# Optimization experiments

Measured on AMD Instinct MI355X. Metric: run time of the kernel, lower is better.

The kernel has to match this reference:

```python
import jax, jax.numpy as jnp
import numpy as np

B, L, D = 4096, 200, 128  # batch, neighbor bonds per molecule, bond feature dim
LN_EPS = 1e-5


def setup_inputs() -> dict:
    key = jax.random.key(0)
    ks = jax.random.split(key, 6)
    s = 1.0 / np.sqrt(D).astype(np.float32)
    return {
        "mol_bond_feature": jax.random.normal(ks[0], (B, D), jnp.float32),
        "bond_feature": jax.random.normal(ks[1], (B, L, D), jnp.float32),
        "mol_bond_attend_mask": jnp.ones((B, L, 1), jnp.float32),
        "mol_bond_softmax_mask": jnp.zeros((B, L, 1), jnp.float32),
        "W_self": jax.random.normal(ks[2], (D, D), jnp.float32) * s,   # mol_bond_fc
        "b_self": jnp.zeros((D,), jnp.float32),
        "W_nb": jax.random.normal(ks[3], (D, D), jnp.float32) * s,     # mol_bond_neighbor_fc
        "b_nb": jnp.zeros((D,), jnp.float32),
        "w_align": jax.random.normal(ks[4], (2 * D,), jnp.float32) * s,  # GAT align weight [2D]->1
        "b_align": jnp.zeros((), jnp.float32),
        "ln_gamma": jnp.ones((D,), jnp.float32),
        "ln_beta": jnp.zeros((D,), jnp.float32),
    }


def reference(mol_bond_feature, bond_feature, mol_bond_attend_mask,
              mol_bond_softmax_mask, W_self, b_self, W_nb, b_nb,
              w_align, b_align, ln_gamma, ln_beta):
    # Linear projections (dropout p=0 -> identity)
    x = mol_bond_feature @ W_self.T + b_self            # [B, D]
    y = jnp.einsum('bld,ed->ble', bond_feature, W_nb) + b_nb  # [B, L, D]

    # GAT align: Linear over concat([x_expand, y]) == split dot products (no concat materialized)
    wx, wy = w_align[:D], w_align[D:]
    score = (x @ wx)[:, None, None] + jnp.einsum('bld,d->bl', y, wy)[..., None] + b_align  # [B, L, 1]
    score = jax.nn.leaky_relu(score)                    # GNN_attn_act
    score = score + mol_bond_softmax_mask

    attn = jax.nn.softmax(score, axis=-2) * mol_bond_attend_mask  # [B, L, 1]
    ctx = jnp.sum(attn * y, axis=-2)                    # [B, D]

    # LayerNorm
    mu = jnp.mean(ctx, axis=-1, keepdims=True)
    var = jnp.mean(jnp.square(ctx - mu), axis=-1, keepdims=True)
    return (ctx - mu) * jax.lax.rsqrt(var + LN_EPS) * ln_gamma + ln_beta
```

## Files before the change

### kernel.cpp

```cpp
#include <hip/hip_runtime.h>
#include <math.h>

#define B_ 4096
#define L_ 200
#define D_ 128

__global__ void prep_kernel(const float* __restrict__ W_self,
                            const float* __restrict__ W_nb,
                            const float* __restrict__ b_self,
                            const float* __restrict__ b_nb,
                            const float* __restrict__ w_align,
                            const float* __restrict__ b_align,
                            float* __restrict__ ws) {
  int d = threadIdx.x;
  float su = 0.f, sv = 0.f;
  for (int e = 0; e < D_; ++e) {
    su = fmaf(w_align[e],      W_self[e * D_ + d], su);
    sv = fmaf(w_align[D_ + e], W_nb[e * D_ + d],   sv);
  }
  ws[d]      = su;
  ws[D_ + d] = sv;
  if (d == 0) {
    float cb = 0.f, cc = 0.f;
    for (int e = 0; e < D_; ++e) {
      cb = fmaf(b_self[e], w_align[e],      cb);
      cc = fmaf(b_nb[e],   w_align[D_ + e], cc);
    }
    ws[2 * D_]     = cb;
    ws[2 * D_ + 1] = cc + b_align[0];
  }
}

__global__ __launch_bounds__(256) void mol_bond_main(
    const float* __restrict__ mbf,
    const float* __restrict__ bond,
    const float* __restrict__ amask,
    const float* __restrict__ smask,
    const float* __restrict__ W_nb,
    const float* __restrict__ b_nb,
    const float* __restrict__ gamma,
    const float* __restrict__ beta,
    const float* __restrict__ ws,
    float* __restrict__ out) {
  const int b    = blockIdx.x;
  const int tid  = threadIdx.x;
  const int w    = tid >> 6;
  const int lane = tid & 63;
  const int half = lane >> 5;
  const int sl   = lane & 31;
  const int d0   = 4 * sl;

  __shared__ float am_s[L_];
  __shared__ float sm_s[L_];
  __shared__ float g_l[8][D_];
  __shared__ float sA[8][2];
  __shared__ float gfin[D_];
  __shared__ float ctx_l[D_];
  __shared__ float Afin_s;

  for (int l = tid; l < L_; l += 256) {
    am_s[l] = amask[(size_t)b * L_ + l];
    sm_s[l] = smask[(size_t)b * L_ + l];
  }

  const float4 uu = *(const float4*)(ws + d0);
  const float4 vv = *(const float4*)(ws + D_ + d0);
  const float  cb = ws[2 * D_], cc = ws[2 * D_ + 1];

  float4 mb = *(const float4*)(mbf + (size_t)b * D_ + d0);
  float xp = mb.x * uu.x + mb.y * uu.y + mb.z * uu.z + mb.w * uu.w;
  xp += __shfl_xor(xp, 16, 64);
  xp += __shfl_xor(xp, 8, 64);
  xp += __shfl_xor(xp, 4, 64);
  xp += __shfl_xor(xp, 2, 64);
  xp += __shfl_xor(xp, 1, 64);
  const float xs = xp + cb;

  __syncthreads();

  float s = 0.f, A = 0.f;
  float g0 = 0.f, g1 = 0.f, g2 = 0.f, g3 = 0.f;
  const float* bb = bond + (size_t)b * (L_ * D_);

  int l = w * 2 + half;
  #pragma unroll 5
  for (int it = 0; it < L_ / 8; ++it, l += 8) {
    float4 f = *(const float4*)(bb + l * D_ + d0);
    float t = f.x * vv.x + f.y * vv.y + f.z * vv.z + f.w * vv.w;
    t += __shfl_xor(t, 16, 64);
    t += __shfl_xor(t, 8, 64);
    t += __shfl_xor(t, 4, 64);
    t += __shfl_xor(t, 2, 64);
    t += __shfl_xor(t, 1, 64);
    float sc = xs + t + cc;
    sc = sc >= 0.f ? sc : 0.01f * sc;
    sc += sm_s[l];
    float p  = __expf(sc);
    float pa = p * am_s[l];
    s += p;
    A += pa;
    g0 = fmaf(pa, f.x, g0);
    g1 = fmaf(pa, f.y, g1);
    g2 = fmaf(pa, f.z, g2);
    g3 = fmaf(pa, f.w, g3);
  }
  const int st = w * 2 + half;
  *(float4*)(&g_l[st][d0]) = make_float4(g0, g1, g2, g3);
  if (sl == 0) { sA[st][0] = s; sA[st][1] = A; }
  __syncthreads();

  if (tid < D_) {
    float gs = 0.f, stot = 0.f, At = 0.f;
    #pragma unroll
    for (int k = 0; k < 8; ++k) {
      gs   += g_l[k][tid];
      stot += sA[k][0];
      At   += sA[k][1];
    }
    float inv = 1.0f / stot;
    gfin[tid] = gs * inv;
    if (tid == 0) Afin_s = At * inv;
  }
  __syncthreads();

  if (tid < D_) {
    const int e = tid;
    const float4* Wr = (const float4*)(W_nb + (size_t)e * D_);
    float acc = b_nb[e] * Afin_s;
    #pragma unroll 8
    for (int k = 0; k < D_ / 4; ++k) {
      float4 wv = Wr[k];
      acc += wv.x * gfin[4 * k]     + wv.y * gfin[4 * k + 1]
           + wv.z * gfin[4 * k + 2] + wv.w * gfin[4 * k + 3];
    }
    ctx_l[e] = acc;
  }
  __syncthreads();

  if (tid < 64) {
    float c0 = ctx_l[lane], c1 = ctx_l[lane + 64];
    float t0 = c0 + c1;
    t0 += __shfl_xor(t0, 32, 64);
    t0 += __shfl_xor(t0, 16, 64);
    t0 += __shfl_xor(t0, 8, 64);
    t0 += __shfl_xor(t0, 4, 64);
    t0 += __shfl_xor(t0, 2, 64);
    t0 += __shfl_xor(t0, 1, 64);
    float mu = t0 * (1.0f / 128.0f);
    float dd0 = c0 - mu, dd1 = c1 - mu;
    float v0 = dd0 * dd0 + dd1 * dd1;
    v0 += __shfl_xor(v0, 32, 64);
    v0 += __shfl_xor(v0, 16, 64);
    v0 += __shfl_xor(v0, 8, 64);
    v0 += __shfl_xor(v0, 4, 64);
    v0 += __shfl_xor(v0, 2, 64);
    v0 += __shfl_xor(v0, 1, 64);
    float var = v0 * (1.0f / 128.0f);
    float inv = rsqrtf(var + 1e-5f);
    out[(size_t)b * D_ + lane]      = dd0 * inv * gamma[lane]      + beta[lane];
    out[(size_t)b * D_ + lane + 64] = dd1 * inv * gamma[lane + 64] + beta[lane + 64];
  }
}

extern "C" void kernel_launch(void* const* d_in, const int* in_sizes, int n_in,
                              void* d_out, int out_size, void* d_ws, size_t ws_size,
                              hipStream_t stream) {
  const float* mbf     = (const float*)d_in[0];
  const float* bond    = (const float*)d_in[1];
  const float* amask   = (const float*)d_in[2];
  const float* smask   = (const float*)d_in[3];
  const float* W_self  = (const float*)d_in[4];
  const float* b_self  = (const float*)d_in[5];
  const float* W_nb    = (const float*)d_in[6];
  const float* b_nb    = (const float*)d_in[7];
  const float* w_align = (const float*)d_in[8];
  const float* b_align = (const float*)d_in[9];
  const float* gamma   = (const float*)d_in[10];
  const float* beta    = (const float*)d_in[11];
  float* ws  = (float*)d_ws;
  float* out = (float*)d_out;

  prep_kernel<<<1, D_, 0, stream>>>(W_self, W_nb, b_self, b_nb, w_align, b_align, ws);
  mol_bond_main<<<B_, 256, 0, stream>>>(mbf, bond, amask, smask, W_nb, b_nb,
                                        gamma, beta, ws, out);
}
```

Before: 103.3 us.

## Split per-molecule W_nb projection and LayerNorm into a batched follow-up kernel

The streaming kernel now only computes the attention-weighted sum of raw bond features and writes it, with the attention mass, to the output and workspace. A new kernel then applies the W_nb projection and LayerNorm to 8 molecules per block, reading a transposed W_nb that the prep kernel builds. Each wave also covers 4 rows of 16 lanes with two float4 loads using nontemporal hints. This removes the serial 128x128 matvec tail from every streaming block, at the cost of an extra launch and an output round trip. The path is chosen only when the workspace is large enough.

```diff
diff --git a/kernel.cpp b/kernel.cpp
--- a/kernel.cpp
+++ b/kernel.cpp
@@ -4,6 +4,12 @@
 #define B_ 4096
 #define L_ 200
 #define D_ 128
+
+typedef float f4 __attribute__((ext_vector_type(4)));
+
+#define WS_AFIN 512
+#define WS_WT   5120
+#define WS_NEED ((size_t)(WS_WT + D_ * D_) * sizeof(float))
 
 __global__ void prep_kernel(const float* __restrict__ W_self,
                             const float* __restrict__ W_nb,
@@ -11,27 +17,34 @@
                             const float* __restrict__ b_nb,
                             const float* __restrict__ w_align,
                             const float* __restrict__ b_align,
-                            float* __restrict__ ws) {
-  int d = threadIdx.x;
-  float su = 0.f, sv = 0.f;
-  for (int e = 0; e < D_; ++e) {
-    su = fmaf(w_align[e],      W_self[e * D_ + d], su);
-    sv = fmaf(w_align[D_ + e], W_nb[e * D_ + d],   sv);
-  }
-  ws[d]      = su;
-  ws[D_ + d] = sv;
-  if (d == 0) {
-    float cb = 0.f, cc = 0.f;
+                            float* __restrict__ ws, int do_wt) {
+  const int blk = blockIdx.x;
+  const int t = threadIdx.x;
+  if (blk == 0) {
+    float su = 0.f, sv = 0.f;
     for (int e = 0; e < D_; ++e) {
-      cb = fmaf(b_self[e], w_align[e],      cb);
-      cc = fmaf(b_nb[e],   w_align[D_ + e], cc);
-    }
-    ws[2 * D_]     = cb;
-    ws[2 * D_ + 1] = cc + b_align[0];
-  }
-}
-
-__global__ __launch_bounds__(256) void mol_bond_main(
+      su = fmaf(w_align[e],      W_self[e * D_ + t], su);
+      sv = fmaf(w_align[D_ + e], W_nb[e * D_ + t],   sv);
+    }
+    ws[t]      = su;
+    ws[D_ + t] = sv;
+    if (t == 0) {
+      float cb = 0.f, cc = 0.f;
+      for (int e = 0; e < D_; ++e) {
+        cb = fmaf(b_self[e], w_align[e],      cb);
+        cc = fmaf(b_nb[e],   w_align[D_ + e], cc);
+      }
+      ws[2 * D_]     = cb;
+      ws[2 * D_ + 1] = cc + b_align[0];
+    }
+  } else if (do_wt) {
+    const int d = blk - 1;
+    ws[WS_WT + d * D_ + t] = W_nb[t * D_ + d];
+  }
+}
+
+template <bool SPLIT>
+__global__ __launch_bounds__(256) void mol_bond_stream(
     const float* __restrict__ mbf,
     const float* __restrict__ bond,
     const float* __restrict__ amask,
@@ -40,126 +53,185 @@
     const float* __restrict__ b_nb,
     const float* __restrict__ gamma,
     const float* __restrict__ beta,
-    const float* __restrict__ ws,
+    float* __restrict__ ws,
     float* __restrict__ out) {
   const int b    = blockIdx.x;
   const int tid  = threadIdx.x;
   const int w    = tid >> 6;
   const int lane = tid & 63;
-  const int half = lane >> 5;
-  const int sl   = lane & 31;
-  const int d0   = 4 * sl;
+  const int g    = lane >> 4;
+  const int sl   = lane & 15;
+  const int dA   = 4 * sl;
+  const int dB   = 64 + 4 * sl;
+  const int rg   = w * 4 + g;
 
   __shared__ float am_s[L_];
   __shared__ float sm_s[L_];
-  __shared__ float g_l[8][D_];
-  __shared__ float sA[8][2];
+  __shared__ float g_l[16][D_];
+  __shared__ float sA[16][2];
   __shared__ float gfin[D_];
   __shared__ float ctx_l[D_];
   __shared__ float Afin_s;
 
-  for (int l = tid; l < L_; l += 256) {
-    am_s[l] = amask[(size_t)b * L_ + l];
-    sm_s[l] = smask[(size_t)b * L_ + l];
-  }
-
-  const float4 uu = *(const float4*)(ws + d0);
-  const float4 vv = *(const float4*)(ws + D_ + d0);
-  const float  cb = ws[2 * D_], cc = ws[2 * D_ + 1];
-
-  float4 mb = *(const float4*)(mbf + (size_t)b * D_ + d0);
-  float xp = mb.x * uu.x + mb.y * uu.y + mb.z * uu.z + mb.w * uu.w;
-  xp += __shfl_xor(xp, 16, 64);
+  for (int l0 = tid; l0 < L_; l0 += 256) {
+    am_s[l0] = amask[(size_t)b * L_ + l0];
+    sm_s[l0] = smask[(size_t)b * L_ + l0];
+  }
+
+  const f4 uA = *(const f4*)(ws + dA);
+  const f4 uB = *(const f4*)(ws + dB);
+  const f4 vA = *(const f4*)(ws + D_ + dA);
+  const f4 vB = *(const f4*)(ws + D_ + dB);
+  const float cb = ws[2 * D_], cc = ws[2 * D_ + 1];
+
+  const f4 mA = *(const f4*)(mbf + (size_t)b * D_ + dA);
+  const f4 mB = *(const f4*)(mbf + (size_t)b * D_ + dB);
+  float xp = mA.x * uA.x + mA.y * uA.y + mA.z * uA.z + mA.w * uA.w
+           + mB.x * uB.x + mB.y * uB.y + mB.z * uB.z + mB.w * uB.w;
   xp += __shfl_xor(xp, 8, 64);
   xp += __shfl_xor(xp, 4, 64);
   xp += __shfl_xor(xp, 2, 64);
   xp += __shfl_xor(xp, 1, 64);
-  const float xs = xp + cb;
+  const float xc = xp + cb + cc;
 
   __syncthreads();
 
   float s = 0.f, A = 0.f;
-  float g0 = 0.f, g1 = 0.f, g2 = 0.f, g3 = 0.f;
+  f4 gA = {0.f, 0.f, 0.f, 0.f};
+  f4 gB = {0.f, 0.f, 0.f, 0.f};
   const float* bb = bond + (size_t)b * (L_ * D_);
 
-  int l = w * 2 + half;
-  #pragma unroll 5
-  for (int it = 0; it < L_ / 8; ++it, l += 8) {
-    float4 f = *(const float4*)(bb + l * D_ + d0);
-    float t = f.x * vv.x + f.y * vv.y + f.z * vv.z + f.w * vv.w;
-    t += __shfl_xor(t, 16, 64);
+  auto body = [&](int l) {
+    f4 fA = __builtin_nontemporal_load((const f4*)(bb + l * D_ + dA));
+    f4 fB = __builtin_nontemporal_load((const f4*)(bb + l * D_ + dB));
+    float t = fA.x * vA.x + fA.y * vA.y + fA.z * vA.z + fA.w * vA.w
+            + fB.x * vB.x + fB.y * vB.y + fB.z * vB.z + fB.w * vB.w;
     t += __shfl_xor(t, 8, 64);
     t += __shfl_xor(t, 4, 64);
     t += __shfl_xor(t, 2, 64);
     t += __shfl_xor(t, 1, 64);
-    float sc = xs + t + cc;
-    sc = sc >= 0.f ? sc : 0.01f * sc;
-    sc += sm_s[l];
-    float p  = __expf(sc);
+    float sc = xc + t;
+    sc = fmaxf(sc, 0.f) + 0.01f * fminf(sc, 0.f);
+    float p  = __expf(sc + sm_s[l]);
     float pa = p * am_s[l];
     s += p;
     A += pa;
-    g0 = fmaf(pa, f.x, g0);
-    g1 = fmaf(pa, f.y, g1);
-    g2 = fmaf(pa, f.z, g2);
-    g3 = fmaf(pa, f.w, g3);
-  }
-  const int st = w * 2 + half;
-  *(float4*)(&g_l[st][d0]) = make_float4(g0, g1, g2, g3);
-  if (sl == 0) { sA[st][0] = s; sA[st][1] = A; }
+    gA.x = fmaf(pa, fA.x, gA.x);
+    gA.y = fmaf(pa, fA.y, gA.y);
+    gA.z = fmaf(pa, fA.z, gA.z);
+    gA.w = fmaf(pa, fA.w, gA.w);
+    gB.x = fmaf(pa, fB.x, gB.x);
+    gB.y = fmaf(pa, fB.y, gB.y);
+    gB.z = fmaf(pa, fB.z, gB.z);
+    gB.w = fmaf(pa, fB.w, gB.w);
+  };
+
+  int l = rg;
+  #pragma unroll 4
+  for (int it = 0; it < 12; ++it, l += 16) body(l);
+  if (rg < 8) body(192 + rg);
+
+  *(f4*)&g_l[rg][dA] = gA;
+  *(f4*)&g_l[rg][dB] = gB;
+  if (sl == 0) { sA[rg][0] = s; sA[rg][1] = A; }
   __syncthreads();
 
   if (tid < D_) {
-    float gs = 0.f, stot = 0.f, At = 0.f;
+    float gs = 0.f, st = 0.f, At = 0.f;
     #pragma unroll
-    for (int k = 0; k < 8; ++k) {
-      gs   += g_l[k][tid];
-      stot += sA[k][0];
-      At   += sA[k][1];
-    }
-    float inv = 1.0f / stot;
-    gfin[tid] = gs * inv;
-    if (tid == 0) Afin_s = At * inv;
-  }
+    for (int k = 0; k < 16; ++k) {
+      gs += g_l[k][tid];
+      st += sA[k][0];
+      At += sA[k][1];
+    }
+    float inv = 1.0f / st;
+    if constexpr (SPLIT) {
+      out[(size_t)b * D_ + tid] = gs * inv;
+      if (tid == 0) ws[WS_AFIN + b] = At * inv;
+    } else {
+      gfin[tid] = gs * inv;
+      if (tid == 0) Afin_s = At * inv;
+    }
+  }
+
+  if constexpr (!SPLIT) {
+    __syncthreads();
+    if (tid < D_) {
+      const int e = tid;
+      const f4* Wr = (const f4*)(W_nb + (size_t)e * D_);
+      float acc = b_nb[e] * Afin_s;
+      #pragma unroll 8
+      for (int k = 0; k < D_ / 4; ++k) {
+        f4 wv = Wr[k];
+        acc += wv.x * gfin[4 * k]     + wv.y * gfin[4 * k + 1]
+             + wv.z * gfin[4 * k + 2] + wv.w * gfin[4 * k + 3];
+      }
+      ctx_l[e] = acc;
+    }
+    __syncthreads();
+    if (tid < 64) {
+      float c0 = ctx_l[lane], c1 = ctx_l[lane + 64];
+      float t0 = c0 + c1;
+      for (int o = 32; o >= 1; o >>= 1) t0 += __shfl_xor(t0, o, 64);
+      float mu = t0 * (1.0f / 128.0f);
+      float dd0 = c0 - mu, dd1 = c1 - mu;
+      float v0 = dd0 * dd0 + dd1 * dd1;
+      for (int o = 32; o >= 1; o >>= 1) v0 += __shfl_xor(v0, o, 64);
+      float inv = rsqrtf(v0 * (1.0f / 128.0f) + 1e-5f);
+      out[(size_t)b * D_ + lane]      = dd0 * inv * gamma[lane]      + beta[lane];
+      out[(size_t)b * D_ + lane + 64] = dd1 * inv * gamma[lane + 64] + beta[lane + 64];
+    }
+  }
+}
+
+__global__ __launch_bounds__(256) void ctx_ln_kernel(
+    const float* __restrict__ b_nb, const float* __restrict__ gamma,
+    const float* __restrict__ beta, const float* __restrict__ ws,
+    float* __restrict__ out) {
+  const int tid  = threadIdx.x;
+  const int slot = tid >> 5;
+  const int st   = tid & 31;
+  const int b0   = blockIdx.x * 8;
+  __shared__ float gq[8][D_];
+  __shared__ float Af[8];
+  for (int i = tid; i < 8 * D_; i += 256)
+    gq[i >> 7][i & 127] = out[(size_t)(b0 + (i >> 7)) * D_ + (i & 127)];
+  if (tid < 8) Af[tid] = ws[WS_AFIN + b0 + tid];
   __syncthreads();
 
-  if (tid < D_) {
-    const int e = tid;
-    const float4* Wr = (const float4*)(W_nb + (size_t)e * D_);
-    float acc = b_nb[e] * Afin_s;
-    #pragma unroll 8
-    for (int k = 0; k < D_ / 4; ++k) {
-      float4 wv = Wr[k];
-      acc += wv.x * gfin[4 * k]     + wv.y * gfin[4 * k + 1]
-           + wv.z * gfin[4 * k + 2] + wv.w * gfin[4 * k + 3];
-    }
-    ctx_l[e] = acc;
-  }
-  __syncthreads();
-
-  if (tid < 64) {
-    float c0 = ctx_l[lane], c1 = ctx_l[lane + 64];
-    float t0 = c0 + c1;
-    t0 += __shfl_xor(t0, 32, 64);
-    t0 += __shfl_xor(t0, 16, 64);
-    t0 += __shfl_xor(t0, 8, 64);
-    t0 += __shfl_xor(t0, 4, 64);
-    t0 += __shfl_xor(t0, 2, 64);
-    t0 += __shfl_xor(t0, 1, 64);
-    float mu = t0 * (1.0f / 128.0f);
-    float dd0 = c0 - mu, dd1 = c1 - mu;
-    float v0 = dd0 * dd0 + dd1 * dd1;
-    v0 += __shfl_xor(v0, 32, 64);
-    v0 += __shfl_xor(v0, 16, 64);
-    v0 += __shfl_xor(v0, 8, 64);
-    v0 += __shfl_xor(v0, 4, 64);
-    v0 += __shfl_xor(v0, 2, 64);
-    v0 += __shfl_xor(v0, 1, 64);
-    float var = v0 * (1.0f / 128.0f);
-    float inv = rsqrtf(var + 1e-5f);
-    out[(size_t)b * D_ + lane]      = dd0 * inv * gamma[lane]      + beta[lane];
-    out[(size_t)b * D_ + lane + 64] = dd1 * inv * gamma[lane + 64] + beta[lane + 64];
-  }
+  const int b  = b0 + slot;
+  const int e0 = 4 * st;
+  f4 bn = *(const f4*)(b_nb + e0);
+  f4 acc = bn * Af[slot];
+  const float* WT = ws + WS_WT;
+  #pragma unroll 8
+  for (int d = 0; d < D_; ++d) {
+    f4 wv = *(const f4*)(WT + d * D_ + e0);
+    float gd = gq[slot][d];
+    acc.x = fmaf(gd, wv.x, acc.x);
+    acc.y = fmaf(gd, wv.y, acc.y);
+    acc.z = fmaf(gd, wv.z, acc.z);
+    acc.w = fmaf(gd, wv.w, acc.w);
+  }
+  float sum = acc.x + acc.y + acc.z + acc.w;
+  sum += __shfl_xor(sum, 16, 64);
+  sum += __shfl_xor(sum, 8, 64);
+  sum += __shfl_xor(sum, 4, 64);
+  sum += __shfl_xor(sum, 2, 64);
+  sum += __shfl_xor(sum, 1, 64);
+  float mu = sum * (1.0f / 128.0f);
+  f4 dd = acc - mu;
+  float vs = dd.x * dd.x + dd.y * dd.y + dd.z * dd.z + dd.w * dd.w;
+  vs += __shfl_xor(vs, 16, 64);
+  vs += __shfl_xor(vs, 8, 64);
+  vs += __shfl_xor(vs, 4, 64);
+  vs += __shfl_xor(vs, 2, 64);
+  vs += __shfl_xor(vs, 1, 64);
+  float inv = rsqrtf(vs * (1.0f / 128.0f) + 1e-5f);
+  f4 ga = *(const f4*)(gamma + e0);
+  f4 be = *(const f4*)(beta + e0);
+  f4 r  = dd * inv * ga + be;
+  *(f4*)(out + (size_t)b * D_ + e0) = r;
 }
 
 extern "C" void kernel_launch(void* const* d_in, const int* in_sizes, int n_in,
@@ -180,7 +252,15 @@
   float* ws  = (float*)d_ws;
   float* out = (float*)d_out;
 
-  prep_kernel<<<1, D_, 0, stream>>>(W_self, W_nb, b_self, b_nb, w_align, b_align, ws);
-  mol_bond_main<<<B_, 256, 0, stream>>>(mbf, bond, amask, smask, W_nb, b_nb,
-                                        gamma, beta, ws, out);
-}
+  const bool split = ws_size >= WS_NEED;
+  prep_kernel<<<1 + D_, D_, 0, stream>>>(W_self, W_nb, b_self, b_nb, w_align,
+                                         b_align, ws, split ? 1 : 0);
+  if (split) {
+    mol_bond_stream<true><<<B_, 256, 0, stream>>>(mbf, bond, amask, smask, W_nb,
+                                                  b_nb, gamma, beta, ws, out);
+    ctx_ln_kernel<<<B_ / 8, 256, 0, stream>>>(b_nb, gamma, beta, ws, out);
+  } else {
+    mol_bond_stream<false><<<B_, 256, 0, stream>>>(mbf, bond, amask, smask, W_nb,
+                                                   b_nb, gamma, beta, ws, out);
+  }
+}
```

Result: faster. 89.50 us (median of 2 runs) (-13.4%).
